# Performance work log

Hardware: AMD Instinct MI355X
Metric: run time of the kernel (lower is better)

The kernel has to match this reference:

```python
import jax, jax.numpy as jnp
import numpy as np

N = 30000      # nodes
E = 480000     # edges (no self loops; GATConv adds them)
IN = 256       # in_features
OUT = 128      # out_features == per-head channels (concat=False)
H = 4          # heads
NEG_SLOPE = 0.2


def setup_inputs() -> dict:
    key = jax.random.key(0)
    k = jax.random.split(key, 6)
    x = jax.random.normal(k[0], (N, IN), dtype=jnp.float32)
    src = jax.random.randint(k[1], (E,), 0, N, dtype=jnp.int32)
    # guarantee no self loops (GATConv would strip them before re-adding)
    off = jax.random.randint(k[2], (E,), 1, N, dtype=jnp.int32)
    dst = (src + off) % N
    edge_index = jnp.stack([src, dst])  # [2, E]
    W = jax.random.normal(k[3], (IN, H * OUT), dtype=jnp.float32) / np.float32(np.sqrt(IN))
    att_src = jax.random.normal(k[4], (H, OUT), dtype=jnp.float32) / np.float32(np.sqrt(OUT))
    att_dst = jax.random.normal(k[5], (H, OUT), dtype=jnp.float32) / np.float32(np.sqrt(OUT))
    bias = jnp.zeros((OUT,), dtype=jnp.float32)
    return {"x": x, "edge_index": edge_index, "W": W,
            "att_src": att_src, "att_dst": att_dst, "bias": bias}


def reference(x, edge_index, W, att_src, att_dst, bias):
    n = x.shape[0]
    # dense projection -> per-head features [N, H, C]
    h = (x @ W).reshape(n, H, OUT)
    a_s = jnp.einsum('nhc,hc->nh', h, att_src)  # [N, H]
    a_d = jnp.einsum('nhc,hc->nh', h, att_dst)  # [N, H]
    # add self loops (GATConv default add_self_loops=True)
    loop = jnp.arange(n, dtype=edge_index.dtype)
    src = jnp.concatenate([edge_index[0], loop])  # [Et]
    dst = jnp.concatenate([edge_index[1], loop])  # [Et]
    # per-edge attention logits + LeakyReLU
    alpha = jax.nn.leaky_relu(a_s[src] + a_d[dst], NEG_SLOPE)  # [Et, H]
    # segment softmax over incoming edges of each dst node
    amax = jax.ops.segment_max(alpha, dst, num_segments=n)      # [N, H]
    ex = jnp.exp(alpha - amax[dst])
    denom = jax.ops.segment_sum(ex, dst, num_segments=n)        # [N, H]
    w = ex / denom[dst]                                          # [Et, H]
    # gather source features, weight, scatter-add to dst
    msg = h[src] * w[:, :, None]                                 # [Et, H, C]
    out = jax.ops.segment_sum(msg, dst, num_segments=n)          # [N, H, C]
    # concat=False -> mean over heads, then bias, then module's tanh
    out = out.mean(axis=1) + bias                                # [N, C]
    return jnp.tanh(out)
```

## Files before the change

### kernel.cpp

```cpp
#include <hip/hip_runtime.h>
#include <math.h>

#define IN_F   256
#define OUT_F  128
#define HEADS  4
#define HD     (HEADS * OUT_F)
#define NEG    0.2f
#define CAP    64

typedef __attribute__((ext_vector_type(8))) short short8;
typedef __attribute__((ext_vector_type(4))) float f32x4;

typedef __attribute__((address_space(1))) const void* gp_t;
typedef __attribute__((address_space(3))) void* lp_t;

static __device__ __forceinline__ ushort f2bf(float f) {
    union { float f; unsigned u; } v; v.f = f;
    unsigned r = (v.u + 0x7FFFu + ((v.u >> 16) & 1u)) >> 16;
    return (ushort)r;
}
static __device__ __forceinline__ float bflo(unsigned u) {
    union { unsigned u; float f; } v; v.u = u << 16; return v.f;
}
static __device__ __forceinline__ float bfhi(unsigned u) {
    union { unsigned u; float f; } v; v.u = u & 0xFFFF0000u; return v.f;
}

__global__ __launch_bounds__(256) void cvt_wt(const float* __restrict__ W,
                                              ushort* __restrict__ WT) {
    int idx = blockIdx.x * blockDim.x + threadIdx.x;
    int n = idx >> 8, k = idx & 255;
    WT[idx] = f2bf(W[k * HD + n]);
}
__global__ __launch_bounds__(256) void calc_va(const float* __restrict__ W,
                                               const float* __restrict__ att_src,
                                               const float* __restrict__ att_dst,
                                               float* __restrict__ va_s,
                                               float* __restrict__ va_d) {
    int idx = blockIdx.x * blockDim.x + threadIdx.x;
    int h = idx >> 8, k = idx & 255;
    const float* wr = W + (size_t)k * HD + h * OUT_F;
    const float* as = att_src + h * OUT_F;
    const float* ad = att_dst + h * OUT_F;
    float ss = 0.f, sd = 0.f;
#pragma unroll 8
    for (int c = 0; c < OUT_F; ++c) {
        float w = wr[c];
        ss = fmaf(w, as[c], ss);
        sd = fmaf(w, ad[c], sd);
    }
    va_s[idx] = ss;
    va_d[idx] = sd;
}

__global__ __launch_bounds__(256) void fused_x(const float* __restrict__ X,
                                               const float* __restrict__ va_s,
                                               const float* __restrict__ va_d,
                                               ushort* __restrict__ Xb,
                                               float* __restrict__ a_s,
                                               float* __restrict__ a_d,
                                               int n_nodes) {
    const int lane = threadIdx.x & 63;
    const int node = blockIdx.x * 4 + (threadIdx.x >> 6);
    if (node >= n_nodes) return;
    float4 v = *(const float4*)(X + (size_t)node * IN_F + lane * 4);
    ushort4 o; o.x = f2bf(v.x); o.y = f2bf(v.y); o.z = f2bf(v.z); o.w = f2bf(v.w);
    *(ushort4*)(Xb + (size_t)node * IN_F + lane * 4) = o;

    float ps[HEADS], pd[HEADS];
#pragma unroll
    for (int hd = 0; hd < HEADS; ++hd) {
        float4 s4 = *(const float4*)(va_s + hd * IN_F + lane * 4);
        float4 d4 = *(const float4*)(va_d + hd * IN_F + lane * 4);
        ps[hd] = v.x * s4.x + v.y * s4.y + v.z * s4.z + v.w * s4.w;
        pd[hd] = v.x * d4.x + v.y * d4.y + v.z * d4.z + v.w * d4.w;
    }
#pragma unroll
    for (int off = 32; off > 0; off >>= 1) {
#pragma unroll
        for (int hd = 0; hd < HEADS; ++hd) {
            ps[hd] += __shfl_xor(ps[hd], off, 64);
            pd[hd] += __shfl_xor(pd[hd], off, 64);
        }
    }
    if (lane == 0) {
        float4 s4 = make_float4(ps[0], ps[1], ps[2], ps[3]);
        float4 d4 = make_float4(pd[0], pd[1], pd[2], pd[3]);
        *(float4*)(a_s + node * 4) = s4;
        *(float4*)(a_d + node * 4) = d4;
    }
}

#define GBM 128
#define GBN 128
#define GBK 32

__global__ __launch_bounds__(256) void gemm_mfma(const ushort* __restrict__ Xb,
                                                 const ushort* __restrict__ WT,
                                                 ushort* __restrict__ Hb,
                                                 int n_nodes) {
    __shared__ ushort As[GBM][GBK];
    __shared__ ushort Bs[GBN][GBK];
    const int tid = threadIdx.x;
    const int m0 = blockIdx.y * GBM;
    const int n0 = blockIdx.x * GBN;
    const int wave = tid >> 6, lane = tid & 63;
    const int wm = (wave & 1) * 64, wn = (wave >> 1) * 64;
    const int l15 = lane & 15, quad = lane >> 4;

    const int rr = lane >> 2;
    const int cg = (lane & 3) ^ ((lane >> 3) & 3);
    const int rA = wave * 16 + rr;
    const ushort* gA0 = Xb + (size_t)(m0 + rA) * IN_F + cg * 8;
    const ushort* gA1 = Xb + (size_t)(m0 + 64 + rA) * IN_F + cg * 8;
    const ushort* gB0 = WT + (size_t)(n0 + rA) * IN_F + cg * 8;
    const ushort* gB1 = WT + (size_t)(n0 + 64 + rA) * IN_F + cg * 8;
    ushort* lA0 = &As[wave * 16][0];
    ushort* lA1 = &As[64 + wave * 16][0];
    ushort* lB0 = &Bs[wave * 16][0];
    ushort* lB1 = &Bs[64 + wave * 16][0];

    f32x4 acc[4][4];
#pragma unroll
    for (int i = 0; i < 4; ++i)
#pragma unroll
        for (int j = 0; j < 4; ++j) acc[i][j] = (f32x4){0.f, 0.f, 0.f, 0.f};

    const int ks = (quad ^ ((l15 >> 1) & 3)) * 8;

    for (int k0 = 0; k0 < IN_F; k0 += GBK) {
        __syncthreads();
        __builtin_amdgcn_global_load_lds((gp_t)(gA0 + k0), (lp_t)lA0, 16, 0, 0);
        __builtin_amdgcn_global_load_lds((gp_t)(gA1 + k0), (lp_t)lA1, 16, 0, 0);
        __builtin_amdgcn_global_load_lds((gp_t)(gB0 + k0), (lp_t)lB0, 16, 0, 0);
        __builtin_amdgcn_global_load_lds((gp_t)(gB1 + k0), (lp_t)lB1, 16, 0, 0);
        __syncthreads();

        short8 af[4], bf_[4];
#pragma unroll
        for (int f = 0; f < 4; ++f) {
            af[f]  = *(const short8*)&As[wm + f * 16 + l15][ks];
            bf_[f] = *(const short8*)&Bs[wn + f * 16 + l15][ks];
        }
#pragma unroll
        for (int fm = 0; fm < 4; ++fm)
#pragma unroll
            for (int fn = 0; fn < 4; ++fn)
                acc[fm][fn] = __builtin_amdgcn_mfma_f32_16x16x32_bf16(
                    af[fm], bf_[fn], acc[fm][fn], 0, 0, 0);
    }

#pragma unroll
    for (int fm = 0; fm < 4; ++fm) {
        int gmb = m0 + wm + fm * 16 + quad * 4;
#pragma unroll
        for (int reg = 0; reg < 4; ++reg) {
            int gm = gmb + reg;
            if (gm < n_nodes) {
#pragma unroll
                for (int fn = 0; fn < 4; ++fn)
                    Hb[(size_t)gm * HD + n0 + wn + fn * 16 + l15] =
                        f2bf(acc[fm][fn][reg]);
            }
        }
    }
}

__global__ __launch_bounds__(256) void transpose_h(const unsigned* __restrict__ Hbu,
                                                   uint4* __restrict__ Hc, int n_nodes) {
    const int lane = threadIdx.x & 63;
    const int n = blockIdx.x * 4 + (threadIdx.x >> 6);
    if (n >= n_nodes) return;
    const unsigned* p = Hbu + (size_t)n * 256;
    uint4 v;
    v.x = p[lane];
    v.y = p[64 + lane];
    v.z = p[128 + lane];
    v.w = p[192 + lane];
    Hc[(size_t)n * 64 + lane] = v;
}

__global__ __launch_bounds__(256) void build_table(const int* __restrict__ src,
                                                   const int* __restrict__ dst,
                                                   int* __restrict__ cursor,
                                                   int* __restrict__ table,
                                                   int n_edges) {
    int e = blockIdx.x * blockDim.x + threadIdx.x;
    if (e >= n_edges) return;
    int d = dst[e];
    int r = atomicAdd(&cursor[d], 1);
    if (r < CAP) table[(size_t)d * CAP + r] = src[e];
}

__global__ __launch_bounds__(256) void gat_agg(const uint4* __restrict__ Hc,
                                               const float* __restrict__ a_s,
                                               const float* __restrict__ a_d,
                                               const int* __restrict__ cursor,
                                               const int* __restrict__ table,
                                               const float* __restrict__ bias,
                                               float* __restrict__ out,
                                               int n_nodes) {
    __shared__ float wsh[4][CAP][4];
    const int wv = threadIdx.x >> 6;
    const int lane = threadIdx.x & 63;
    const int n = blockIdx.x * 4 + wv;
    const bool valid = n < n_nodes;

    int deg = 0;
    const int* row = table;
    float es[4], rdv[4];
    if (valid) {
        deg = cursor[n]; if (deg > CAP) deg = CAP;
        row = table + (size_t)n * CAP;

        const float4 ad4 = *(const float4*)(a_d + n * 4);
        const float4 as4 = *(const float4*)(a_s + n * 4);
        const float ad[4] = {ad4.x, ad4.y, ad4.z, ad4.w};
        float aself[4];
        {
            const float asn[4] = {as4.x, as4.y, as4.z, as4.w};
#pragma unroll
            for (int hd = 0; hd < 4; ++hd) {
                float al = asn[hd] + ad[hd];
                aself[hd] = al > 0.f ? al : NEG * al;
            }
        }
        const bool act = lane < deg;
        float al[4];
        {
            int s = act ? row[lane] : 0;
            float4 av = *(const float4*)(a_s + s * 4);
            const float as_[4] = {av.x, av.y, av.z, av.w};
#pragma unroll
            for (int hd = 0; hd < 4; ++hd) {
                float a = as_[hd] + ad[hd];
                a = a > 0.f ? a : NEG * a;
                al[hd] = act ? a : -1e30f;
            }
        }
        float m[4];
#pragma unroll
        for (int hd = 0; hd < 4; ++hd) m[hd] = al[hd];
#pragma unroll
        for (int off = 32; off > 0; off >>= 1)
#pragma unroll
            for (int hd = 0; hd < 4; ++hd)
                m[hd] = fmaxf(m[hd], __shfl_xor(m[hd], off, 64));
#pragma unroll
        for (int hd = 0; hd < 4; ++hd) m[hd] = fmaxf(m[hd], aself[hd]);

        float w[4], den[4];
#pragma unroll
        for (int hd = 0; hd < 4; ++hd) {
            w[hd] = act ? __expf(al[hd] - m[hd]) : 0.f;
            den[hd] = w[hd];
        }
#pragma unroll
        for (int off = 32; off > 0; off >>= 1)
#pragma unroll
            for (int hd = 0; hd < 4; ++hd)
                den[hd] += __shfl_xor(den[hd], off, 64);
#pragma unroll
        for (int hd = 0; hd < 4; ++hd) {
            es[hd] = __expf(aself[hd] - m[hd]);
            rdv[hd] = 1.f / (den[hd] + es[hd]);
        }
        *(float4*)&wsh[wv][lane][0] = make_float4(w[0], w[1], w[2], w[3]);
    }
    __syncthreads();
    if (!valid) return;

    float acc0[4], acc1[4];
    {
        uint4 u = Hc[(size_t)n * 64 + lane];
        acc0[0] = es[0] * bflo(u.x); acc1[0] = es[0] * bfhi(u.x);
        acc0[1] = es[1] * bflo(u.y); acc1[1] = es[1] * bfhi(u.y);
        acc0[2] = es[2] * bflo(u.z); acc1[2] = es[2] * bfhi(u.z);
        acc0[3] = es[3] * bflo(u.w); acc1[3] = es[3] * bfhi(u.w);
    }
    int e = 0;
    for (; e + 8 <= deg; e += 8) {
        int4 ra = *(const int4*)(row + e);
        int4 rb = *(const int4*)(row + e + 4);
        uint4 u[8];
        u[0] = Hc[(size_t)ra.x * 64 + lane];
        u[1] = Hc[(size_t)ra.y * 64 + lane];
        u[2] = Hc[(size_t)ra.z * 64 + lane];
        u[3] = Hc[(size_t)ra.w * 64 + lane];
        u[4] = Hc[(size_t)rb.x * 64 + lane];
        u[5] = Hc[(size_t)rb.y * 64 + lane];
        u[6] = Hc[(size_t)rb.z * 64 + lane];
        u[7] = Hc[(size_t)rb.w * 64 + lane];
#pragma unroll
        for (int j = 0; j < 8; ++j) {
            float4 w4 = *(const float4*)&wsh[wv][e + j][0];
            acc0[0] = fmaf(w4.x, bflo(u[j].x), acc0[0]);
            acc1[0] = fmaf(w4.x, bfhi(u[j].x), acc1[0]);
            acc0[1] = fmaf(w4.y, bflo(u[j].y), acc0[1]);
            acc1[1] = fmaf(w4.y, bfhi(u[j].y), acc1[1]);
            acc0[2] = fmaf(w4.z, bflo(u[j].z), acc0[2]);
            acc1[2] = fmaf(w4.z, bfhi(u[j].z), acc1[2]);
            acc0[3] = fmaf(w4.w, bflo(u[j].w), acc0[3]);
            acc1[3] = fmaf(w4.w, bfhi(u[j].w), acc1[3]);
        }
    }
    for (; e < deg; ++e) {
        int s = row[e];
        uint4 u = Hc[(size_t)s * 64 + lane];
        float4 w4 = *(const float4*)&wsh[wv][e][0];
        acc0[0] = fmaf(w4.x, bflo(u.x), acc0[0]);
        acc1[0] = fmaf(w4.x, bfhi(u.x), acc1[0]);
        acc0[1] = fmaf(w4.y, bflo(u.y), acc0[1]);
        acc1[1] = fmaf(w4.y, bfhi(u.y), acc1[1]);
        acc0[2] = fmaf(w4.z, bflo(u.z), acc0[2]);
        acc1[2] = fmaf(w4.z, bfhi(u.z), acc1[2]);
        acc0[3] = fmaf(w4.w, bflo(u.w), acc0[3]);
        acc1[3] = fmaf(w4.w, bfhi(u.w), acc1[3]);
    }
    float o0 = 0.f, o1 = 0.f;
#pragma unroll
    for (int hd = 0; hd < 4; ++hd) {
        o0 = fmaf(acc0[hd], rdv[hd], o0);
        o1 = fmaf(acc1[hd], rdv[hd], o1);
    }
    float2 b = *(const float2*)(bias + 2 * lane);
    o0 = 0.25f * o0 + b.x;
    o1 = 0.25f * o1 + b.y;
    float2 ov = make_float2(tanhf(o0), tanhf(o1));
    *(float2*)(out + (size_t)n * OUT_F + 2 * lane) = ov;
}

extern "C" void kernel_launch(void* const* d_in, const int* in_sizes, int n_in,
                              void* d_out, int out_size, void* d_ws, size_t ws_size,
                              hipStream_t stream) {
    const float* x       = (const float*)d_in[0];
    const int*   ei      = (const int*)d_in[1];
    const float* W       = (const float*)d_in[2];
    const float* att_src = (const float*)d_in[3];
    const float* att_dst = (const float*)d_in[4];
    const float* bias    = (const float*)d_in[5];
    float* out = (float*)d_out;

    const int n_nodes = in_sizes[0] / IN_F;
    const int n_edges = in_sizes[1] / 2;
    const int* src = ei;
    const int* dst = ei + n_edges;

    char* ws = (char*)d_ws;
    size_t off = 0;
    auto alloc = [&](size_t bytes) -> void* {
        void* p = ws + off;
        off = (off + bytes + 255) & ~(size_t)255;
        return p;
    };
    ushort* Xb     = (ushort*)alloc((size_t)n_nodes * IN_F * sizeof(ushort));
    ushort* Hb     = (ushort*)alloc((size_t)n_nodes * HD * sizeof(ushort));
    uint4*  Hc     = (uint4*)alloc((size_t)n_nodes * 64 * sizeof(uint4));
    ushort* WT     = (ushort*)alloc((size_t)HD * IN_F * sizeof(ushort));
    float*  va_s   = (float*)alloc((size_t)HEADS * IN_F * sizeof(float));
    float*  va_d   = (float*)alloc((size_t)HEADS * IN_F * sizeof(float));
    float*  a_s    = (float*)alloc((size_t)n_nodes * HEADS * sizeof(float));
    float*  a_d    = (float*)alloc((size_t)n_nodes * HEADS * sizeof(float));
    int*    cursor = (int*)alloc((size_t)n_nodes * sizeof(int));
    int*    table  = (int*)alloc((size_t)n_nodes * CAP * sizeof(int));
    (void)ws_size; (void)n_in; (void)out_size;

    hipMemsetAsync(cursor, 0, (size_t)n_nodes * sizeof(int), stream);

    cvt_wt<<<(HD * IN_F) / 256, 256, 0, stream>>>(W, WT);
    calc_va<<<(HEADS * IN_F) / 256, 256, 0, stream>>>(W, att_src, att_dst, va_s, va_d);
    fused_x<<<(n_nodes + 3) / 4, 256, 0, stream>>>(x, va_s, va_d, Xb, a_s, a_d, n_nodes);
    build_table<<<(n_edges + 255) / 256, 256, 0, stream>>>(src, dst, cursor, table, n_edges);

    dim3 ggrid(HD / GBN, (n_nodes + GBM - 1) / GBM);
    gemm_mfma<<<ggrid, 256, 0, stream>>>(Xb, WT, Hb, n_nodes);
    transpose_h<<<(n_nodes + 3) / 4, 256, 0, stream>>>((const unsigned*)Hb, Hc, n_nodes);

    gat_agg<<<(n_nodes + 3) / 4, 256, 0, stream>>>(Hc, a_s, a_d, cursor, table,
                                                   bias, out, n_nodes);
}
```

Before: 235.6 us.

## Write interleaved head layout from GEMM epilogue and drop transpose kernel

Result: slower. 247.9 us (+5.2%).

```diff
diff --git a/kernel.cpp b/kernel.cpp
--- a/kernel.cpp
+++ b/kernel.cpp
@@ -97,13 +97,14 @@
 
 __global__ __launch_bounds__(256) void gemm_mfma(const ushort* __restrict__ Xb,
                                                  const ushort* __restrict__ WT,
-                                                 ushort* __restrict__ Hb,
+                                                 ushort* __restrict__ HcU,
                                                  int n_nodes) {
     __shared__ ushort As[GBM][GBK];
     __shared__ ushort Bs[GBN][GBK];
     const int tid = threadIdx.x;
     const int m0 = blockIdx.y * GBM;
     const int n0 = blockIdx.x * GBN;
+    const int head = blockIdx.x;
     const int wave = tid >> 6, lane = tid & 63;
     const int wm = (wave & 1) * 64, wn = (wave >> 1) * 64;
     const int l15 = lane & 15, quad = lane >> 4;
@@ -158,26 +159,14 @@
             int gm = gmb + reg;
             if (gm < n_nodes) {
 #pragma unroll
-                for (int fn = 0; fn < 4; ++fn)
-                    Hb[(size_t)gm * HD + n0 + wn + fn * 16 + l15] =
+                for (int fn = 0; fn < 4; ++fn) {
+                    int ch = wn + fn * 16 + l15;
+                    HcU[(size_t)gm * 512 + (ch >> 1) * 8 + head * 2 + (ch & 1)] =
                         f2bf(acc[fm][fn][reg]);
+                }
             }
         }
     }
-}
-
-__global__ __launch_bounds__(256) void transpose_h(const unsigned* __restrict__ Hbu,
-                                                   uint4* __restrict__ Hc, int n_nodes) {
-    const int lane = threadIdx.x & 63;
-    const int n = blockIdx.x * 4 + (threadIdx.x >> 6);
-    if (n >= n_nodes) return;
-    const unsigned* p = Hbu + (size_t)n * 256;
-    uint4 v;
-    v.x = p[lane];
-    v.y = p[64 + lane];
-    v.z = p[128 + lane];
-    v.w = p[192 + lane];
-    Hc[(size_t)n * 64 + lane] = v;
 }
 
 __global__ __launch_bounds__(256) void build_table(const int* __restrict__ src,
@@ -197,78 +186,71 @@
                                                const float* __restrict__ a_d,
                                                const int* __restrict__ cursor,
                                                const int* __restrict__ table,
+                                               float* wtab,
                                                const float* __restrict__ bias,
                                                float* __restrict__ out,
                                                int n_nodes) {
-    __shared__ float wsh[4][CAP][4];
-    const int wv = threadIdx.x >> 6;
     const int lane = threadIdx.x & 63;
-    const int n = blockIdx.x * 4 + wv;
-    const bool valid = n < n_nodes;
-
-    int deg = 0;
-    const int* row = table;
-    float es[4], rdv[4];
-    if (valid) {
-        deg = cursor[n]; if (deg > CAP) deg = CAP;
-        row = table + (size_t)n * CAP;
-
-        const float4 ad4 = *(const float4*)(a_d + n * 4);
-        const float4 as4 = *(const float4*)(a_s + n * 4);
-        const float ad[4] = {ad4.x, ad4.y, ad4.z, ad4.w};
-        float aself[4];
-        {
-            const float asn[4] = {as4.x, as4.y, as4.z, as4.w};
-#pragma unroll
-            for (int hd = 0; hd < 4; ++hd) {
-                float al = asn[hd] + ad[hd];
-                aself[hd] = al > 0.f ? al : NEG * al;
-            }
-        }
-        const bool act = lane < deg;
-        float al[4];
-        {
-            int s = act ? row[lane] : 0;
-            float4 av = *(const float4*)(a_s + s * 4);
-            const float as_[4] = {av.x, av.y, av.z, av.w};
-#pragma unroll
-            for (int hd = 0; hd < 4; ++hd) {
-                float a = as_[hd] + ad[hd];
-                a = a > 0.f ? a : NEG * a;
-                al[hd] = act ? a : -1e30f;
-            }
-        }
-        float m[4];
-#pragma unroll
-        for (int hd = 0; hd < 4; ++hd) m[hd] = al[hd];
-#pragma unroll
-        for (int off = 32; off > 0; off >>= 1)
-#pragma unroll
-            for (int hd = 0; hd < 4; ++hd)
-                m[hd] = fmaxf(m[hd], __shfl_xor(m[hd], off, 64));
-#pragma unroll
-        for (int hd = 0; hd < 4; ++hd) m[hd] = fmaxf(m[hd], aself[hd]);
-
-        float w[4], den[4];
+    const int n = blockIdx.x * 4 + (threadIdx.x >> 6);
+    if (n >= n_nodes) return;
+    int deg = cursor[n]; if (deg > CAP) deg = CAP;
+    const int* row = table + (size_t)n * CAP;
+    float* wrow = wtab + (size_t)n * CAP * 4;
+
+    const float4 ad4 = *(const float4*)(a_d + n * 4);
+    const float4 as4 = *(const float4*)(a_s + n * 4);
+    const float ad[4] = {ad4.x, ad4.y, ad4.z, ad4.w};
+    float aself[4];
+    {
+        const float asn[4] = {as4.x, as4.y, as4.z, as4.w};
 #pragma unroll
         for (int hd = 0; hd < 4; ++hd) {
-            w[hd] = act ? __expf(al[hd] - m[hd]) : 0.f;
-            den[hd] = w[hd];
-        }
-#pragma unroll
-        for (int off = 32; off > 0; off >>= 1)
-#pragma unroll
-            for (int hd = 0; hd < 4; ++hd)
-                den[hd] += __shfl_xor(den[hd], off, 64);
+            float al = asn[hd] + ad[hd];
+            aself[hd] = al > 0.f ? al : NEG * al;
+        }
+    }
+    const bool act = lane < deg;
+    float al[4];
+    {
+        int s = act ? row[lane] : 0;
+        float4 av = *(const float4*)(a_s + s * 4);
+        const float as_[4] = {av.x, av.y, av.z, av.w};
 #pragma unroll
         for (int hd = 0; hd < 4; ++hd) {
-            es[hd] = __expf(aself[hd] - m[hd]);
-            rdv[hd] = 1.f / (den[hd] + es[hd]);
-        }
-        *(float4*)&wsh[wv][lane][0] = make_float4(w[0], w[1], w[2], w[3]);
-    }
-    __syncthreads();
-    if (!valid) return;
+            float a = as_[hd] + ad[hd];
+            a = a > 0.f ? a : NEG * a;
+            al[hd] = act ? a : -1e30f;
+        }
+    }
+    float m[4];
+#pragma unroll
+    for (int hd = 0; hd < 4; ++hd) m[hd] = al[hd];
+#pragma unroll
+    for (int off = 32; off > 0; off >>= 1)
+#pragma unroll
+        for (int hd = 0; hd < 4; ++hd)
+            m[hd] = fmaxf(m[hd], __shfl_xor(m[hd], off, 64));
+#pragma unroll
+    for (int hd = 0; hd < 4; ++hd) m[hd] = fmaxf(m[hd], aself[hd]);
+
+    float w[4], den[4], es[4], rdv[4];
+#pragma unroll
+    for (int hd = 0; hd < 4; ++hd) {
+        w[hd] = act ? __expf(al[hd] - m[hd]) : 0.f;
+        den[hd] = w[hd];
+    }
+#pragma unroll
+    for (int off = 32; off > 0; off >>= 1)
+#pragma unroll
+        for (int hd = 0; hd < 4; ++hd)
+            den[hd] += __shfl_xor(den[hd], off, 64);
+#pragma unroll
+    for (int hd = 0; hd < 4; ++hd) {
+        es[hd] = __expf(aself[hd] - m[hd]);
+        rdv[hd] = 1.f / (den[hd] + es[hd]);
+    }
+    if (act)
+        *(float4*)(wrow + lane * 4) = make_float4(w[0], w[1], w[2], w[3]);
 
     float acc0[4], acc1[4];
     {
@@ -293,7 +275,7 @@
         u[7] = Hc[(size_t)rb.w * 64 + lane];
 #pragma unroll
         for (int j = 0; j < 8; ++j) {
-            float4 w4 = *(const float4*)&wsh[wv][e + j][0];
+            float4 w4 = *(const float4*)(wrow + (e + j) * 4);
             acc0[0] = fmaf(w4.x, bflo(u[j].x), acc0[0]);
             acc1[0] = fmaf(w4.x, bfhi(u[j].x), acc1[0]);
             acc0[1] = fmaf(w4.y, bflo(u[j].y), acc0[1]);
@@ -307,7 +289,7 @@
     for (; e < deg; ++e) {
         int s = row[e];
         uint4 u = Hc[(size_t)s * 64 + lane];
-        float4 w4 = *(const float4*)&wsh[wv][e][0];
+        float4 w4 = *(const float4*)(wrow + e * 4);
         acc0[0] = fmaf(w4.x, bflo(u.x), acc0[0]);
         acc1[0] = fmaf(w4.x, bfhi(u.x), acc1[0]);
         acc0[1] = fmaf(w4.y, bflo(u.y), acc0[1]);
@@ -354,7 +336,6 @@
         return p;
     };
     ushort* Xb     = (ushort*)alloc((size_t)n_nodes * IN_F * sizeof(ushort));
-    ushort* Hb     = (ushort*)alloc((size_t)n_nodes * HD * sizeof(ushort));
     uint4*  Hc     = (uint4*)alloc((size_t)n_nodes * 64 * sizeof(uint4));
     ushort* WT     = (ushort*)alloc((size_t)HD * IN_F * sizeof(ushort));
     float*  va_s   = (float*)alloc((size_t)HEADS * IN_F * sizeof(float));
@@ -363,6 +344,7 @@
     float*  a_d    = (float*)alloc((size_t)n_nodes * HEADS * sizeof(float));
     int*    cursor = (int*)alloc((size_t)n_nodes * sizeof(int));
     int*    table  = (int*)alloc((size_t)n_nodes * CAP * sizeof(int));
+    float*  wtab   = (float*)alloc((size_t)n_nodes * CAP * 4 * sizeof(float));
     (void)ws_size; (void)n_in; (void)out_size;
 
     hipMemsetAsync(cursor, 0, (size_t)n_nodes * sizeof(int), stream);
@@ -373,9 +355,8 @@
     build_table<<<(n_edges + 255) / 256, 256, 0, stream>>>(src, dst, cursor, table, n_edges);
 
     dim3 ggrid(HD / GBN, (n_nodes + GBM - 1) / GBM);
-    gemm_mfma<<<ggrid, 256, 0, stream>>>(Xb, WT, Hb, n_nodes);
-    transpose_h<<<(n_nodes + 3) / 4, 256, 0, stream>>>((const unsigned*)Hb, Hc, n_nodes);
+    gemm_mfma<<<ggrid, 256, 0, stream>>>(Xb, WT, (ushort*)Hc, n_nodes);
 
     gat_agg<<<(n_nodes + 3) / 4, 256, 0, stream>>>(Hc, a_s, a_d, cursor, table,
-                                                   bias, out, n_nodes);
-}
+                                                   wtab, bias, out, n_nodes);
+}
```
